# Optimization experiments

Hardware: AMD Instinct MI355X
Metric: run time of the kernel (lower is better)

Reference implementation:

```python
import jax, jax.numpy as jnp
import numpy as np

D_MODEL = 1024
NHEAD = 16
HEAD_DIM = D_MODEL // NHEAD
EPS = 1e-6


def setup_inputs() -> dict:
    key = jax.random.key(0)
    ks = jax.random.split(key, 9)
    B, S = 2, 2048
    scale = 1.0 / np.sqrt(D_MODEL)
    inp = {
        "x": jax.random.normal(ks[0], (B, S, D_MODEL), dtype=jnp.float32),
        "wq": jax.random.normal(ks[1], (D_MODEL, D_MODEL), dtype=jnp.float32) * scale,
        "bq": jnp.zeros((D_MODEL,), dtype=jnp.float32),
        "wk": jax.random.normal(ks[2], (D_MODEL, D_MODEL), dtype=jnp.float32) * scale,
        "bk": jnp.zeros((D_MODEL,), dtype=jnp.float32),
        "wv": jax.random.normal(ks[3], (D_MODEL, D_MODEL), dtype=jnp.float32) * scale,
        "bv": jnp.zeros((D_MODEL,), dtype=jnp.float32),
        "wo": jax.random.normal(ks[4], (D_MODEL, D_MODEL), dtype=jnp.float32) * scale,
        "bo": jnp.zeros((D_MODEL,), dtype=jnp.float32),
    }
    return inp


def _split_heads(x):
    B, S, _ = x.shape
    return x.reshape(B, S, NHEAD, HEAD_DIM).transpose(0, 2, 1, 3)  # [B,H,S,Dh]


def reference(x, wq, bq, wk, bk, wv, bv, wo, bo):
    # projections (torch Linear: x @ W^T + b)
    q = _split_heads(x @ wq.T + bq)
    k = _split_heads(x @ wk.T + bk)
    v = _split_heads(x @ wv.T + bv)
    # positive feature map: elu(x) + 1
    q_feat = jax.nn.elu(q) + 1.0
    k_feat = jax.nn.elu(k) + 1.0
    # dense O(n^2) kernelized scores, per original module
    scores = jnp.einsum('bhid,bhjd->bhij', q_feat, k_feat)
    denom = jnp.maximum(scores.sum(axis=-1, keepdims=True), EPS)
    weights = scores / denom  # dropout p=0 -> identity
    attended = jnp.einsum('bhij,bhjd->bhid', weights, v)
    B, H, S, Dh = attended.shape
    merged = attended.transpose(0, 2, 1, 3).reshape(B, S, H * Dh)
    return merged @ wo.T + bo
```

## Files before the change

### kernel.cpp

```cpp
#include <hip/hip_runtime.h>
#include <math.h>

#define S_LEN 2048
#define BATCH 2
#define DM 1024
#define NH 16
#define DH 64
#define EPS 1e-6f

typedef __attribute__((ext_vector_type(8))) short bf16x8;
typedef __attribute__((ext_vector_type(4))) float f32x4;

__device__ __forceinline__ unsigned short f2bf(float f) {
    unsigned u = __float_as_uint(f);
    u = (u + 0x7fffu + ((u >> 16) & 1u)) >> 16;
    return (unsigned short)u;
}
__device__ __forceinline__ float2 bf2f2(unsigned u) {
    float2 r;
    r.x = __uint_as_float(u << 16);
    r.y = __uint_as_float(u & 0xFFFF0000u);
    return r;
}
__device__ __forceinline__ void unpack8(uint4 u, float* f) {
    float2 a = bf2f2(u.x), b = bf2f2(u.y), c = bf2f2(u.z), d = bf2f2(u.w);
    f[0] = a.x; f[1] = a.y; f[2] = b.x; f[3] = b.y;
    f[4] = c.x; f[5] = c.y; f[6] = d.x; f[7] = d.y;
}
__device__ __forceinline__ void load16(const void* g, void* l) {
    __builtin_amdgcn_global_load_lds(
        (const __attribute__((address_space(1))) unsigned int*)g,
        (__attribute__((address_space(3))) unsigned int*)l,
        16, 0, 0);
}

__global__ __launch_bounds__(256) void cvt5_bf16(
    const float* __restrict__ s0, const float* __restrict__ s1,
    const float* __restrict__ s2, const float* __restrict__ s3,
    const float* __restrict__ s4,
    unsigned short* __restrict__ d0, unsigned short* __restrict__ d1,
    unsigned short* __restrict__ d2, unsigned short* __restrict__ d3,
    unsigned short* __restrict__ d4,
    int n8_x, int n8_w)
{
    const int z = blockIdx.y;
    const float* s = (z == 0) ? s0 : (z == 1) ? s1 : (z == 2) ? s2 : (z == 3) ? s3 : s4;
    unsigned short* d = (z == 0) ? d0 : (z == 1) ? d1 : (z == 2) ? d2 : (z == 3) ? d3 : d4;
    const int n8 = (z == 0) ? n8_x : n8_w;
    int i = blockIdx.x * 256 + threadIdx.x;
    if (i >= n8) return;
    float4 a = ((const float4*)s)[2 * i];
    float4 b = ((const float4*)s)[2 * i + 1];
    uint4 o;
    o.x = (unsigned)f2bf(a.x) | ((unsigned)f2bf(a.y) << 16);
    o.y = (unsigned)f2bf(a.z) | ((unsigned)f2bf(a.w) << 16);
    o.z = (unsigned)f2bf(b.x) | ((unsigned)f2bf(b.y) << 16);
    o.w = (unsigned)f2bf(b.z) | ((unsigned)f2bf(b.w) << 16);
    ((uint4*)d)[i] = o;
}

template <int OUTF32>
__global__ __launch_bounds__(256) void gemm_mfma(
    const unsigned short* __restrict__ A,
    const unsigned short* __restrict__ W0, const unsigned short* __restrict__ W1,
    const unsigned short* __restrict__ W2,
    const float* __restrict__ B0, const float* __restrict__ B1, const float* __restrict__ B2,
    void* __restrict__ O0, void* __restrict__ O1, void* __restrict__ O2,
    int M, int N, int K, int act_mask)
{
    const int z = blockIdx.z;
    const unsigned short* W = (z == 0) ? W0 : (z == 1) ? W1 : W2;
    const float* bias       = (z == 0) ? B0 : (z == 1) ? B1 : B2;
    void* O                 = (z == 0) ? O0 : (z == 1) ? O1 : O2;
    const bool act = (act_mask >> z) & 1;

    __shared__ __align__(16) unsigned short AsU[128 * 32];
    __shared__ __align__(16) unsigned short BsU[128 * 32];

    const int tid = threadIdx.x;
    const int wave = tid >> 6;
    const int lane = tid & 63;
    const int quad = lane >> 4;
    const int lm = lane & 15;
    const int wr = wave >> 1, wc = wave & 1;

    const int rowBase = blockIdx.y * 128;
    const int colBase = blockIdx.x * 128;

    const int s0 = wave * 128 + lane, s1 = s0 + 64;
    const int ra0 = s0 >> 2, ca0 = (s0 & 3) ^ ((ra0 >> 1) & 3);
    const int ra1 = s1 >> 2, ca1 = (s1 & 3) ^ ((ra1 >> 1) & 3);
    const unsigned short* Ag0 = A + (size_t)(rowBase + ra0) * K + ca0 * 8;
    const unsigned short* Ag1 = A + (size_t)(rowBase + ra1) * K + ca1 * 8;
    const unsigned short* Wg0 = W + (size_t)(colBase + ra0) * K + ca0 * 8;
    const unsigned short* Wg1 = W + (size_t)(colBase + ra1) * K + ca1 * 8;
    unsigned short* lA0 = AsU + (size_t)(wave * 128) * 8;
    unsigned short* lA1 = AsU + (size_t)(wave * 128 + 64) * 8;
    unsigned short* lB0 = BsU + (size_t)(wave * 128) * 8;
    unsigned short* lB1 = BsU + (size_t)(wave * 128 + 64) * 8;

    const unsigned short* pA[4];
    const unsigned short* pB[4];
#pragma unroll
    for (int i = 0; i < 4; ++i) {
        int r = wr * 64 + i * 16 + lm;
        int cp = quad ^ ((r >> 1) & 3);
        pA[i] = AsU + (size_t)(r * 4 + cp) * 8;
        int n = wc * 64 + i * 16 + lm;
        int cq = quad ^ ((n >> 1) & 3);
        pB[i] = BsU + (size_t)(n * 4 + cq) * 8;
    }

    f32x4 acc[4][4];
#pragma unroll
    for (int i = 0; i < 4; ++i)
#pragma unroll
        for (int j = 0; j < 4; ++j)
            acc[i][j] = (f32x4){0.f, 0.f, 0.f, 0.f};

    for (int k0 = 0; k0 < K; k0 += 32) {
        load16(Ag0 + k0, lA0);
        load16(Ag1 + k0, lA1);
        load16(Wg0 + k0, lB0);
        load16(Wg1 + k0, lB1);
        __syncthreads();
        bf16x8 aF[4], bF[4];
#pragma unroll
        for (int i = 0; i < 4; ++i) {
            aF[i] = *(const bf16x8*)pA[i];
            bF[i] = *(const bf16x8*)pB[i];
        }
#pragma unroll
        for (int i = 0; i < 4; ++i)
#pragma unroll
            for (int j = 0; j < 4; ++j)
                acc[i][j] = __builtin_amdgcn_mfma_f32_16x16x32_bf16(aF[i], bF[j], acc[i][j], 0, 0, 0);
        __syncthreads();
    }

#pragma unroll
    for (int j = 0; j < 4; ++j) {
        const int col = colBase + wc * 64 + j * 16 + lm;
        const float bc = bias[col];
#pragma unroll
        for (int i = 0; i < 4; ++i) {
            const int row0 = rowBase + wr * 64 + i * 16 + quad * 4;
#pragma unroll
            for (int reg = 0; reg < 4; ++reg) {
                float v = acc[i][j][reg] + bc;
                if (act) v = (v > 0.0f) ? (v + 1.0f) : __expf(v);
                size_t idx = (size_t)(row0 + reg) * N + col;
                if (OUTF32) ((float*)O)[idx] = v;
                else ((unsigned short*)O)[idx] = f2bf(v);
            }
        }
    }
}

__global__ __launch_bounds__(256) void kv_part_kernel(
    const unsigned short* __restrict__ kf, const unsigned short* __restrict__ vv,
    float* __restrict__ kv_part, float* __restrict__ ksum_part)
{
    const int bh = blockIdx.x;
    const int b = bh >> 4, h = bh & 15;
    const int tid = threadIdx.x;
    const int wave = tid >> 6, lane = tid & 63;
    const int p = blockIdx.y * 4 + wave;
    const int posBase = p * 128;

    __shared__ __align__(16) float Ks[4][2][16][68];
    __shared__ __align__(16) float Vs[4][2][16][68];

    const int pos_l = lane >> 3;
    const int f0 = (lane & 7) * 8;
    const int r0 = pos_l * 8;
    const int c0 = f0;

    float acc[8][8] = {};
    float srow[8] = {};

    for (int st = 0; st < 8; ++st) {
        const int buf = st & 1;
        size_t g0 = ((size_t)(b * S_LEN + posBase + st * 16 + pos_l)) * DM + h * DH + f0;
        size_t g1 = g0 + (size_t)8 * DM;
        uint4 ka = *(const uint4*)(kf + g0);
        uint4 kb = *(const uint4*)(kf + g1);
        uint4 va = *(const uint4*)(vv + g0);
        uint4 vb = *(const uint4*)(vv + g1);
        float kaf[8], kbf[8], vaf[8], vbf[8];
        unpack8(ka, kaf); unpack8(kb, kbf); unpack8(va, vaf); unpack8(vb, vbf);
#pragma unroll
        for (int j = 0; j < 8; ++j) srow[j] += kaf[j] + kbf[j];
        *(float4*)&Ks[wave][buf][pos_l][f0]         = make_float4(kaf[0], kaf[1], kaf[2], kaf[3]);
        *(float4*)&Ks[wave][buf][pos_l][f0 + 4]     = make_float4(kaf[4], kaf[5], kaf[6], kaf[7]);
        *(float4*)&Ks[wave][buf][pos_l + 8][f0]     = make_float4(kbf[0], kbf[1], kbf[2], kbf[3]);
        *(float4*)&Ks[wave][buf][pos_l + 8][f0 + 4] = make_float4(kbf[4], kbf[5], kbf[6], kbf[7]);
        *(float4*)&Vs[wave][buf][pos_l][f0]         = make_float4(vaf[0], vaf[1], vaf[2], vaf[3]);
        *(float4*)&Vs[wave][buf][pos_l][f0 + 4]     = make_float4(vaf[4], vaf[5], vaf[6], vaf[7]);
        *(float4*)&Vs[wave][buf][pos_l + 8][f0]     = make_float4(vbf[0], vbf[1], vbf[2], vbf[3]);
        *(float4*)&Vs[wave][buf][pos_l + 8][f0 + 4] = make_float4(vbf[4], vbf[5], vbf[6], vbf[7]);
#pragma unroll 4
        for (int q = 0; q < 16; ++q) {
            float4 a0 = *(const float4*)&Ks[wave][buf][q][r0];
            float4 a1 = *(const float4*)&Ks[wave][buf][q][r0 + 4];
            float4 b0 = *(const float4*)&Vs[wave][buf][q][c0];
            float4 b1 = *(const float4*)&Vs[wave][buf][q][c0 + 4];
            float aa[8] = {a0.x, a0.y, a0.z, a0.w, a1.x, a1.y, a1.z, a1.w};
            float bb[8] = {b0.x, b0.y, b0.z, b0.w, b1.x, b1.y, b1.z, b1.w};
#pragma unroll
            for (int i = 0; i < 8; ++i)
#pragma unroll
                for (int j = 0; j < 8; ++j)
                    acc[i][j] += aa[i] * bb[j];
        }
    }

#pragma unroll
    for (int j = 0; j < 8; ++j) {
        srow[j] += __shfl_xor(srow[j], 8);
        srow[j] += __shfl_xor(srow[j], 16);
        srow[j] += __shfl_xor(srow[j], 32);
    }

    float* kvp = kv_part + ((size_t)bh * 16 + p) * (DH * DH);
#pragma unroll
    for (int j = 0; j < 8; ++j) {
        *(float4*)&kvp[(c0 + j) * DH + r0] =
            make_float4(acc[0][j], acc[1][j], acc[2][j], acc[3][j]);
        *(float4*)&kvp[(c0 + j) * DH + r0 + 4] =
            make_float4(acc[4][j], acc[5][j], acc[6][j], acc[7][j]);
    }
    if (pos_l == 0) {
        float* ksp = ksum_part + ((size_t)bh * 16 + p) * DH + f0;
        *(float4*)&ksp[0] = make_float4(srow[0], srow[1], srow[2], srow[3]);
        *(float4*)&ksp[4] = make_float4(srow[4], srow[5], srow[6], srow[7]);
    }
}

__global__ __launch_bounds__(256) void kv_reduce_kernel(
    const float* __restrict__ kv_part, const float* __restrict__ ksum_part,
    unsigned short* __restrict__ kvT_bf, float* __restrict__ ksum)
{
    const int bh = blockIdx.x;
    const int tid = threadIdx.x;
    float s[16] = {};
    const float* base = kv_part + (size_t)bh * 16 * (DH * DH) + tid * 16;
#pragma unroll 4
    for (int p = 0; p < 16; ++p) {
        const float4* b4 = (const float4*)(base + (size_t)p * (DH * DH));
#pragma unroll
        for (int q = 0; q < 4; ++q) {
            float4 v = b4[q];
            s[q * 4 + 0] += v.x; s[q * 4 + 1] += v.y;
            s[q * 4 + 2] += v.z; s[q * 4 + 3] += v.w;
        }
    }
    unsigned short us[16];
#pragma unroll
    for (int i = 0; i < 16; ++i) us[i] = f2bf(s[i]);
    uint4 o0, o1;
    o0.x = (unsigned)us[0]  | ((unsigned)us[1]  << 16);
    o0.y = (unsigned)us[2]  | ((unsigned)us[3]  << 16);
    o0.z = (unsigned)us[4]  | ((unsigned)us[5]  << 16);
    o0.w = (unsigned)us[6]  | ((unsigned)us[7]  << 16);
    o1.x = (unsigned)us[8]  | ((unsigned)us[9]  << 16);
    o1.y = (unsigned)us[10] | ((unsigned)us[11] << 16);
    o1.z = (unsigned)us[12] | ((unsigned)us[13] << 16);
    o1.w = (unsigned)us[14] | ((unsigned)us[15] << 16);
    uint4* dst = (uint4*)(kvT_bf + (size_t)bh * (DH * DH) + tid * 16);
    dst[0] = o0; dst[1] = o1;
    if (tid < DH) {
        float t = 0.f;
#pragma unroll 4
        for (int p = 0; p < 16; ++p)
            t += ksum_part[((size_t)bh * 16 + p) * DH + tid];
        ksum[bh * DH + tid] = t;
    }
}

__global__ __launch_bounds__(256) void attend_mfma(
    const unsigned short* __restrict__ qf, const unsigned short* __restrict__ kvT_bf,
    const float* __restrict__ ksum, unsigned short* __restrict__ att)
{
    const int sBase = blockIdx.x * 128;
    const int bh = blockIdx.y;
    const int b = bh >> 4, h = bh & 15;

    __shared__ __align__(16) unsigned short Qs[128 * 64];
    __shared__ __align__(16) unsigned short Ts[64 * 64];
    __shared__ __align__(16) float ks_s[DH];
    __shared__ float den_s[128];

    const int tid = threadIdx.x;
    const int wave = tid >> 6, lane = tid & 63;
    const int quad = lane >> 4, lm = lane & 15;

#pragma unroll
    for (int i = 0; i < 4; ++i) {
        int slot = (wave * 4 + i) * 64 + lane;
        int r = slot >> 3;
        int c = (slot & 7) ^ (r & 7);
        const unsigned short* src =
            qf + ((size_t)(b * S_LEN + sBase + r)) * DM + h * DH + c * 8;
        load16(src, Qs + (size_t)(wave * 4 + i) * 512);
    }
#pragma unroll
    for (int i = 0; i < 2; ++i) {
        int slot = (wave * 2 + i) * 64 + lane;
        int e = slot >> 3;
        int c = (slot & 7) ^ (e & 7);
        const unsigned short* src = kvT_bf + (size_t)bh * (DH * DH) + e * DH + c * 8;
        load16(src, Ts + (size_t)(wave * 2 + i) * 512);
    }
    if (tid < 16)
        *(float4*)&ks_s[tid * 4] = *(const float4*)&ksum[bh * DH + tid * 4];
    __syncthreads();

    if (tid < 128) {
        const int r = tid;
        float d = 0.f;
#pragma unroll
        for (int cxx = 0; cxx < 8; ++cxx) {
            int slot = r * 8 + (cxx ^ (r & 7));
            uint4 u = *(const uint4*)(Qs + slot * 8);
            float f[8]; unpack8(u, f);
            const float* kss = &ks_s[cxx * 8];
#pragma unroll
            for (int j = 0; j < 8; ++j) d += f[j] * kss[j];
        }
        den_s[r] = fmaxf(d, EPS);
    }
    __syncthreads();

    f32x4 acc[2][4];
#pragma unroll
    for (int ti = 0; ti < 2; ++ti)
#pragma unroll
        for (int tj = 0; tj < 4; ++tj)
            acc[ti][tj] = (f32x4){0.f, 0.f, 0.f, 0.f};

#pragma unroll
    for (int ks_i = 0; ks_i < 2; ++ks_i) {
        bf16x8 aF[2], bF[4];
#pragma unroll
        for (int ti = 0; ti < 2; ++ti) {
            int r = wave * 32 + ti * 16 + lm;
            int cx = (ks_i * 4 + quad) ^ (r & 7);
            aF[ti] = *(const bf16x8*)(Qs + (r * 8 + cx) * 8);
        }
#pragma unroll
        for (int tj = 0; tj < 4; ++tj) {
            int e = tj * 16 + lm;
            int cx = (ks_i * 4 + quad) ^ (e & 7);
            bF[tj] = *(const bf16x8*)(Ts + (e * 8 + cx) * 8);
        }
#pragma unroll
        for (int ti = 0; ti < 2; ++ti)
#pragma unroll
            for (int tj = 0; tj < 4; ++tj)
                acc[ti][tj] = __builtin_amdgcn_mfma_f32_16x16x32_bf16(aF[ti], bF[tj], acc[ti][tj], 0, 0, 0);
    }

#pragma unroll
    for (int ti = 0; ti < 2; ++ti) {
        const int rloc0 = wave * 32 + ti * 16 + quad * 4;
#pragma unroll
        for (int reg = 0; reg < 4; ++reg) {
            float inv = 1.0f / den_s[rloc0 + reg];
            unsigned short* dst =
                att + ((size_t)(b * S_LEN + sBase + rloc0 + reg)) * DM + h * DH;
#pragma unroll
            for (int tj = 0; tj < 4; ++tj)
                dst[tj * 16 + lm] = f2bf(acc[ti][tj][reg] * inv);
        }
    }
}

extern "C" void kernel_launch(void* const* d_in, const int* in_sizes, int n_in,
                              void* d_out, int out_size, void* d_ws, size_t ws_size,
                              hipStream_t stream) {
    const float* x  = (const float*)d_in[0];
    const float* wq = (const float*)d_in[1];
    const float* bq = (const float*)d_in[2];
    const float* wk = (const float*)d_in[3];
    const float* bk = (const float*)d_in[4];
    const float* wv = (const float*)d_in[5];
    const float* bv = (const float*)d_in[6];
    const float* wo = (const float*)d_in[7];
    const float* bo = (const float*)d_in[8];
    float* out = (float*)d_out;

    const size_t ND  = (size_t)BATCH * S_LEN * DM;
    const size_t NDW = (size_t)DM * DM;
    const int BH = BATCH * NH;

    unsigned short* x_bf   = (unsigned short*)d_ws;
    unsigned short* wq_bf  = x_bf + ND;
    unsigned short* wk_bf  = wq_bf + NDW;
    unsigned short* wv_bf  = wk_bf + NDW;
    unsigned short* wo_bf  = wv_bf + NDW;
    unsigned short* qf_bf  = wo_bf + NDW;
    unsigned short* kf_bf  = qf_bf + ND;
    unsigned short* vv_bf  = kf_bf + ND;
    unsigned short* att_bf = vv_bf + ND;
    unsigned short* kvT_bf = att_bf + ND;
    float* kv_part   = (float*)(kvT_bf + (size_t)BH * DH * DH);
    float* ksum_part = kv_part + (size_t)BH * 16 * DH * DH;
    float* ksum      = ksum_part + (size_t)BH * 16 * DH;

    const int M = BATCH * S_LEN;
    const int n8x = (int)(ND / 8), n8w = (int)(NDW / 8);

    cvt5_bf16<<<dim3(n8x / 256, 5), 256, 0, stream>>>(
        x, wq, wk, wv, wo, x_bf, wq_bf, wk_bf, wv_bf, wo_bf, n8x, n8w);

    gemm_mfma<0><<<dim3(DM / 128, M / 128, 3), 256, 0, stream>>>(
        x_bf, wq_bf, wk_bf, wv_bf, bq, bk, bv,
        (void*)qf_bf, (void*)kf_bf, (void*)vv_bf, M, DM, DM, 0b011);

    kv_part_kernel<<<dim3(BH, 4), 256, 0, stream>>>(kf_bf, vv_bf, kv_part, ksum_part);

    kv_reduce_kernel<<<BH, 256, 0, stream>>>(kv_part, ksum_part, kvT_bf, ksum);

    attend_mfma<<<dim3(S_LEN / 128, BH), 256, 0, stream>>>(qf_bf, kvT_bf, ksum, att_bf);

    gemm_mfma<1><<<dim3(DM / 128, M / 128, 1), 256, 0, stream>>>(
        att_bf, wo_bf, wo_bf, wo_bf, bo, bo, bo,
        (void*)out, (void*)out, (void*)out, M, DM, DM, 0);
}
```

Before: 191.3 us.

## Fuse KV reduction into partial and attend kernels, retile output GEMM

The kv partials are now reduced across the four waves in shared memory inside kv_part_kernel, so only 4 partials per head are written instead of 16. The final 4-way sum, bf16 conversion and swizzled store into shared memory move into attend_mfma, which removes the separate kv_reduce launch. The output projection gets its own 64x128-tile GEMM kernel so the grid has twice as many blocks. The weight/x conversion becomes a single flat 1D launch. In exchange, every attend block re-reduces the partials redundantly, and the smaller output tiles lower data reuse per block.

```diff
diff --git a/kernel.cpp b/kernel.cpp
--- a/kernel.cpp
+++ b/kernel.cpp
@@ -34,44 +34,50 @@
         16, 0, 0);
 }
 
-__global__ __launch_bounds__(256) void cvt5_bf16(
-    const float* __restrict__ s0, const float* __restrict__ s1,
-    const float* __restrict__ s2, const float* __restrict__ s3,
-    const float* __restrict__ s4,
-    unsigned short* __restrict__ d0, unsigned short* __restrict__ d1,
-    unsigned short* __restrict__ d2, unsigned short* __restrict__ d3,
-    unsigned short* __restrict__ d4,
-    int n8_x, int n8_w)
+__global__ __launch_bounds__(256) void cvt_flat(
+    const float* __restrict__ x,
+    const float* __restrict__ wq, const float* __restrict__ wk,
+    const float* __restrict__ wv, const float* __restrict__ wo,
+    unsigned short* __restrict__ x_bf,
+    unsigned short* __restrict__ wq_bf, unsigned short* __restrict__ wk_bf,
+    unsigned short* __restrict__ wv_bf, unsigned short* __restrict__ wo_bf)
 {
-    const int z = blockIdx.y;
-    const float* s = (z == 0) ? s0 : (z == 1) ? s1 : (z == 2) ? s2 : (z == 3) ? s3 : s4;
-    unsigned short* d = (z == 0) ? d0 : (z == 1) ? d1 : (z == 2) ? d2 : (z == 3) ? d3 : d4;
-    const int n8 = (z == 0) ? n8_x : n8_w;
-    int i = blockIdx.x * 256 + threadIdx.x;
-    if (i >= n8) return;
-    float4 a = ((const float4*)s)[2 * i];
-    float4 b = ((const float4*)s)[2 * i + 1];
+    int u = blockIdx.x * 256 + threadIdx.x;
+    const float* s;
+    unsigned short* d;
+    int off;
+    if (u < 524288) {
+        s = x; d = x_bf; off = u;
+    } else {
+        int v = u - 524288;
+        int w = v >> 17;
+        off = v & 131071;
+        s = (w == 0) ? wq : (w == 1) ? wk : (w == 2) ? wv : wo;
+        d = (w == 0) ? wq_bf : (w == 1) ? wk_bf : (w == 2) ? wv_bf : wo_bf;
+    }
+    float4 a = ((const float4*)s)[2 * off];
+    float4 b = ((const float4*)s)[2 * off + 1];
     uint4 o;
     o.x = (unsigned)f2bf(a.x) | ((unsigned)f2bf(a.y) << 16);
     o.y = (unsigned)f2bf(a.z) | ((unsigned)f2bf(a.w) << 16);
     o.z = (unsigned)f2bf(b.x) | ((unsigned)f2bf(b.y) << 16);
     o.w = (unsigned)f2bf(b.z) | ((unsigned)f2bf(b.w) << 16);
-    ((uint4*)d)[i] = o;
-}
-
-template <int OUTF32>
-__global__ __launch_bounds__(256) void gemm_mfma(
+    ((uint4*)d)[off] = o;
+}
+
+__global__ __launch_bounds__(256) void gemm_qkv(
     const unsigned short* __restrict__ A,
     const unsigned short* __restrict__ W0, const unsigned short* __restrict__ W1,
     const unsigned short* __restrict__ W2,
     const float* __restrict__ B0, const float* __restrict__ B1, const float* __restrict__ B2,
-    void* __restrict__ O0, void* __restrict__ O1, void* __restrict__ O2,
+    unsigned short* __restrict__ O0, unsigned short* __restrict__ O1,
+    unsigned short* __restrict__ O2,
     int M, int N, int K, int act_mask)
 {
     const int z = blockIdx.z;
     const unsigned short* W = (z == 0) ? W0 : (z == 1) ? W1 : W2;
     const float* bias       = (z == 0) ? B0 : (z == 1) ? B1 : B2;
-    void* O                 = (z == 0) ? O0 : (z == 1) ? O1 : O2;
+    unsigned short* O       = (z == 0) ? O0 : (z == 1) ? O1 : O2;
     const bool act = (act_mask >> z) & 1;
 
     __shared__ __align__(16) unsigned short AsU[128 * 32];
@@ -149,10 +155,93 @@
             for (int reg = 0; reg < 4; ++reg) {
                 float v = acc[i][j][reg] + bc;
                 if (act) v = (v > 0.0f) ? (v + 1.0f) : __expf(v);
-                size_t idx = (size_t)(row0 + reg) * N + col;
-                if (OUTF32) ((float*)O)[idx] = v;
-                else ((unsigned short*)O)[idx] = f2bf(v);
+                O[(size_t)(row0 + reg) * N + col] = f2bf(v);
             }
+        }
+    }
+}
+
+__global__ __launch_bounds__(256) void gemm_out(
+    const unsigned short* __restrict__ A,
+    const unsigned short* __restrict__ W,
+    const float* __restrict__ bias,
+    float* __restrict__ O, int M, int N, int K)
+{
+    __shared__ __align__(16) unsigned short AsU[64 * 32];
+    __shared__ __align__(16) unsigned short BsU[128 * 32];
+
+    const int tid = threadIdx.x;
+    const int wave = tid >> 6;
+    const int lane = tid & 63;
+    const int quad = lane >> 4;
+    const int lm = lane & 15;
+    const int wr = wave >> 1, wc = wave & 1;
+
+    const int rowBase = blockIdx.y * 64;
+    const int colBase = blockIdx.x * 128;
+
+    const int sA = tid;
+    const int rA = sA >> 2, cA = (sA & 3) ^ ((rA >> 1) & 3);
+    const unsigned short* Ag = A + (size_t)(rowBase + rA) * K + cA * 8;
+    unsigned short* lA = AsU + (size_t)(wave * 64) * 8;
+    const int s0 = wave * 128 + lane, s1 = s0 + 64;
+    const int rb0 = s0 >> 2, cb0 = (s0 & 3) ^ ((rb0 >> 1) & 3);
+    const int rb1 = s1 >> 2, cb1 = (s1 & 3) ^ ((rb1 >> 1) & 3);
+    const unsigned short* Wg0 = W + (size_t)(colBase + rb0) * K + cb0 * 8;
+    const unsigned short* Wg1 = W + (size_t)(colBase + rb1) * K + cb1 * 8;
+    unsigned short* lB0 = BsU + (size_t)(wave * 128) * 8;
+    unsigned short* lB1 = BsU + (size_t)(wave * 128 + 64) * 8;
+
+    const unsigned short* pA[2];
+    const unsigned short* pB[4];
+#pragma unroll
+    for (int i = 0; i < 2; ++i) {
+        int r = wr * 32 + i * 16 + lm;
+        int cp = quad ^ ((r >> 1) & 3);
+        pA[i] = AsU + (size_t)(r * 4 + cp) * 8;
+    }
+#pragma unroll
+    for (int j = 0; j < 4; ++j) {
+        int n = wc * 64 + j * 16 + lm;
+        int cq = quad ^ ((n >> 1) & 3);
+        pB[j] = BsU + (size_t)(n * 4 + cq) * 8;
+    }
+
+    f32x4 acc[2][4];
+#pragma unroll
+    for (int i = 0; i < 2; ++i)
+#pragma unroll
+        for (int j = 0; j < 4; ++j)
+            acc[i][j] = (f32x4){0.f, 0.f, 0.f, 0.f};
+
+    for (int k0 = 0; k0 < K; k0 += 32) {
+        load16(Ag + k0, lA);
+        load16(Wg0 + k0, lB0);
+        load16(Wg1 + k0, lB1);
+        __syncthreads();
+        bf16x8 aF[2], bF[4];
+#pragma unroll
+        for (int i = 0; i < 2; ++i) aF[i] = *(const bf16x8*)pA[i];
+#pragma unroll
+        for (int j = 0; j < 4; ++j) bF[j] = *(const bf16x8*)pB[j];
+#pragma unroll
+        for (int i = 0; i < 2; ++i)
+#pragma unroll
+            for (int j = 0; j < 4; ++j)
+                acc[i][j] = __builtin_amdgcn_mfma_f32_16x16x32_bf16(aF[i], bF[j], acc[i][j], 0, 0, 0);
+        __syncthreads();
+    }
+
+#pragma unroll
+    for (int j = 0; j < 4; ++j) {
+        const int col = colBase + wc * 64 + j * 16 + lm;
+        const float bc = bias[col];
+#pragma unroll
+        for (int i = 0; i < 2; ++i) {
+            const int row0 = rowBase + wr * 32 + i * 16 + quad * 4;
+#pragma unroll
+            for (int reg = 0; reg < 4; ++reg)
+                O[(size_t)(row0 + reg) * N + col] = acc[i][j][reg] + bc;
         }
     }
 }
@@ -165,11 +254,12 @@
     const int b = bh >> 4, h = bh & 15;
     const int tid = threadIdx.x;
     const int wave = tid >> 6, lane = tid & 63;
-    const int p = blockIdx.y * 4 + wave;
-    const int posBase = p * 128;
-
-    __shared__ __align__(16) float Ks[4][2][16][68];
-    __shared__ __align__(16) float Vs[4][2][16][68];
+    const int blk = blockIdx.y;
+    const int posBase = (blk * 4 + wave) * 128;
+
+    __shared__ __align__(16) float smem[17408];
+    float (*Ks)[2][16][68] = (float (*)[2][16][68])smem;
+    float (*Vs)[2][16][68] = (float (*)[2][16][68])(smem + 8704);
 
     const int pos_l = lane >> 3;
     const int f0 = (lane & 7) * 8;
@@ -222,65 +312,45 @@
         srow[j] += __shfl_xor(srow[j], 32);
     }
 
-    float* kvp = kv_part + ((size_t)bh * 16 + p) * (DH * DH);
+    __syncthreads();
+    float* red = smem;
+    float* ksred = smem + 16384;
 #pragma unroll
     for (int j = 0; j < 8; ++j) {
-        *(float4*)&kvp[(c0 + j) * DH + r0] =
+        *(float4*)&red[wave * 4096 + (c0 + j) * 64 + r0] =
             make_float4(acc[0][j], acc[1][j], acc[2][j], acc[3][j]);
-        *(float4*)&kvp[(c0 + j) * DH + r0 + 4] =
+        *(float4*)&red[wave * 4096 + (c0 + j) * 64 + r0 + 4] =
             make_float4(acc[4][j], acc[5][j], acc[6][j], acc[7][j]);
     }
     if (pos_l == 0) {
-        float* ksp = ksum_part + ((size_t)bh * 16 + p) * DH + f0;
-        *(float4*)&ksp[0] = make_float4(srow[0], srow[1], srow[2], srow[3]);
-        *(float4*)&ksp[4] = make_float4(srow[4], srow[5], srow[6], srow[7]);
-    }
-}
-
-__global__ __launch_bounds__(256) void kv_reduce_kernel(
-    const float* __restrict__ kv_part, const float* __restrict__ ksum_part,
-    unsigned short* __restrict__ kvT_bf, float* __restrict__ ksum)
-{
-    const int bh = blockIdx.x;
-    const int tid = threadIdx.x;
-    float s[16] = {};
-    const float* base = kv_part + (size_t)bh * 16 * (DH * DH) + tid * 16;
-#pragma unroll 4
-    for (int p = 0; p < 16; ++p) {
-        const float4* b4 = (const float4*)(base + (size_t)p * (DH * DH));
-#pragma unroll
-        for (int q = 0; q < 4; ++q) {
-            float4 v = b4[q];
-            s[q * 4 + 0] += v.x; s[q * 4 + 1] += v.y;
-            s[q * 4 + 2] += v.z; s[q * 4 + 3] += v.w;
-        }
-    }
-    unsigned short us[16];
-#pragma unroll
-    for (int i = 0; i < 16; ++i) us[i] = f2bf(s[i]);
-    uint4 o0, o1;
-    o0.x = (unsigned)us[0]  | ((unsigned)us[1]  << 16);
-    o0.y = (unsigned)us[2]  | ((unsigned)us[3]  << 16);
-    o0.z = (unsigned)us[4]  | ((unsigned)us[5]  << 16);
-    o0.w = (unsigned)us[6]  | ((unsigned)us[7]  << 16);
-    o1.x = (unsigned)us[8]  | ((unsigned)us[9]  << 16);
-    o1.y = (unsigned)us[10] | ((unsigned)us[11] << 16);
-    o1.z = (unsigned)us[12] | ((unsigned)us[13] << 16);
-    o1.w = (unsigned)us[14] | ((unsigned)us[15] << 16);
-    uint4* dst = (uint4*)(kvT_bf + (size_t)bh * (DH * DH) + tid * 16);
-    dst[0] = o0; dst[1] = o1;
-    if (tid < DH) {
-        float t = 0.f;
-#pragma unroll 4
-        for (int p = 0; p < 16; ++p)
-            t += ksum_part[((size_t)bh * 16 + p) * DH + tid];
-        ksum[bh * DH + tid] = t;
+        *(float4*)&ksred[wave * 64 + f0]     = make_float4(srow[0], srow[1], srow[2], srow[3]);
+        *(float4*)&ksred[wave * 64 + f0 + 4] = make_float4(srow[4], srow[5], srow[6], srow[7]);
+    }
+    __syncthreads();
+
+    float* outp = kv_part + ((size_t)bh * 4 + blk) * 4096;
+    const int base = tid * 16;
+#pragma unroll
+    for (int g = 0; g < 4; ++g) {
+        float4 s0 = *(const float4*)&red[base + g * 4];
+        float4 s1 = *(const float4*)&red[4096 + base + g * 4];
+        float4 s2 = *(const float4*)&red[8192 + base + g * 4];
+        float4 s3 = *(const float4*)&red[12288 + base + g * 4];
+        float4 o = make_float4(s0.x + s1.x + s2.x + s3.x,
+                               s0.y + s1.y + s2.y + s3.y,
+                               s0.z + s1.z + s2.z + s3.z,
+                               s0.w + s1.w + s2.w + s3.w);
+        *(float4*)&outp[base + g * 4] = o;
+    }
+    if (tid < 64) {
+        float t = ksred[tid] + ksred[64 + tid] + ksred[128 + tid] + ksred[192 + tid];
+        ksum_part[((size_t)bh * 4 + blk) * 64 + tid] = t;
     }
 }
 
 __global__ __launch_bounds__(256) void attend_mfma(
-    const unsigned short* __restrict__ qf, const unsigned short* __restrict__ kvT_bf,
-    const float* __restrict__ ksum, unsigned short* __restrict__ att)
+    const unsigned short* __restrict__ qf, const float* __restrict__ kv_part,
+    const float* __restrict__ ksum_part, unsigned short* __restrict__ att)
 {
     const int sBase = blockIdx.x * 128;
     const int bh = blockIdx.y;
@@ -304,16 +374,42 @@
             qf + ((size_t)(b * S_LEN + sBase + r)) * DM + h * DH + c * 8;
         load16(src, Qs + (size_t)(wave * 4 + i) * 512);
     }
-#pragma unroll
-    for (int i = 0; i < 2; ++i) {
-        int slot = (wave * 2 + i) * 64 + lane;
-        int e = slot >> 3;
-        int c = (slot & 7) ^ (e & 7);
-        const unsigned short* src = kvT_bf + (size_t)bh * (DH * DH) + e * DH + c * 8;
-        load16(src, Ts + (size_t)(wave * 2 + i) * 512);
-    }
-    if (tid < 16)
-        *(float4*)&ks_s[tid * 4] = *(const float4*)&ksum[bh * DH + tid * 4];
+
+    {
+        const int e = tid >> 2, c2 = tid & 3;
+        const float* kp = kv_part + (size_t)bh * 4 * 4096 + e * 64 + c2 * 16;
+        float s[16];
+#pragma unroll
+        for (int g = 0; g < 4; ++g) {
+            float4 p0 = *(const float4*)(kp + g * 4);
+            float4 p1 = *(const float4*)(kp + 4096 + g * 4);
+            float4 p2 = *(const float4*)(kp + 8192 + g * 4);
+            float4 p3 = *(const float4*)(kp + 12288 + g * 4);
+            s[g * 4 + 0] = p0.x + p1.x + p2.x + p3.x;
+            s[g * 4 + 1] = p0.y + p1.y + p2.y + p3.y;
+            s[g * 4 + 2] = p0.z + p1.z + p2.z + p3.z;
+            s[g * 4 + 3] = p0.w + p1.w + p2.w + p3.w;
+        }
+        unsigned short us[16];
+#pragma unroll
+        for (int i = 0; i < 16; ++i) us[i] = f2bf(s[i]);
+        uint4 lo, hi;
+        lo.x = (unsigned)us[0]  | ((unsigned)us[1]  << 16);
+        lo.y = (unsigned)us[2]  | ((unsigned)us[3]  << 16);
+        lo.z = (unsigned)us[4]  | ((unsigned)us[5]  << 16);
+        lo.w = (unsigned)us[6]  | ((unsigned)us[7]  << 16);
+        hi.x = (unsigned)us[8]  | ((unsigned)us[9]  << 16);
+        hi.y = (unsigned)us[10] | ((unsigned)us[11] << 16);
+        hi.z = (unsigned)us[12] | ((unsigned)us[13] << 16);
+        hi.w = (unsigned)us[14] | ((unsigned)us[15] << 16);
+        const int cL = c2 * 2, cH = c2 * 2 + 1;
+        *(uint4*)(Ts + (size_t)(e * 8 + (cL ^ (e & 7))) * 8) = lo;
+        *(uint4*)(Ts + (size_t)(e * 8 + (cH ^ (e & 7))) * 8) = hi;
+    }
+    if (tid < 64) {
+        const float* kq = ksum_part + (size_t)bh * 4 * 64 + tid;
+        ks_s[tid] = kq[0] + kq[64] + kq[128] + kq[192];
+    }
     __syncthreads();
 
     if (tid < 128) {
@@ -403,28 +499,22 @@
     unsigned short* kf_bf  = qf_bf + ND;
     unsigned short* vv_bf  = kf_bf + ND;
     unsigned short* att_bf = vv_bf + ND;
-    unsigned short* kvT_bf = att_bf + ND;
-    float* kv_part   = (float*)(kvT_bf + (size_t)BH * DH * DH);
-    float* ksum_part = kv_part + (size_t)BH * 16 * DH * DH;
-    float* ksum      = ksum_part + (size_t)BH * 16 * DH;
+    float* kv_part   = (float*)(att_bf + ND);
+    float* ksum_part = kv_part + (size_t)BH * 4 * 4096;
 
     const int M = BATCH * S_LEN;
-    const int n8x = (int)(ND / 8), n8w = (int)(NDW / 8);
-
-    cvt5_bf16<<<dim3(n8x / 256, 5), 256, 0, stream>>>(
-        x, wq, wk, wv, wo, x_bf, wq_bf, wk_bf, wv_bf, wo_bf, n8x, n8w);
-
-    gemm_mfma<0><<<dim3(DM / 128, M / 128, 3), 256, 0, stream>>>(
+
+    cvt_flat<<<4096, 256, 0, stream>>>(x, wq, wk, wv, wo,
+                                       x_bf, wq_bf, wk_bf, wv_bf, wo_bf);
+
+    gemm_qkv<<<dim3(DM / 128, M / 128, 3), 256, 0, stream>>>(
         x_bf, wq_bf, wk_bf, wv_bf, bq, bk, bv,
-        (void*)qf_bf, (void*)kf_bf, (void*)vv_bf, M, DM, DM, 0b011);
+        qf_bf, kf_bf, vv_bf, M, DM, DM, 0b011);
 
     kv_part_kernel<<<dim3(BH, 4), 256, 0, stream>>>(kf_bf, vv_bf, kv_part, ksum_part);
 
-    kv_reduce_kernel<<<BH, 256, 0, stream>>>(kv_part, ksum_part, kvT_bf, ksum);
-
-    attend_mfma<<<dim3(S_LEN / 128, BH), 256, 0, stream>>>(qf_bf, kvT_bf, ksum, att_bf);
-
-    gemm_mfma<1><<<dim3(DM / 128, M / 128, 1), 256, 0, stream>>>(
-        att_bf, wo_bf, wo_bf, wo_bf, bo, bo, bo,
-        (void*)out, (void*)out, (void*)out, M, DM, DM, 0);
-}
+    attend_mfma<<<dim3(S_LEN / 128, BH), 256, 0, stream>>>(qf_bf, kv_part, ksum_part, att_bf);
+
+    gemm_out<<<dim3(DM / 128, M / 64), 256, 0, stream>>>(
+        att_bf, wo_bf, bo, out, M, DM, DM);
+}
```

After: 180.5 us. -5.6%, faster.
